# Kernel tuning notes

Measured on AMD Instinct MI355X. Metric: run time of the kernel, lower is better.

The kernel has to match this reference:

```python
import jax, jax.numpy as jnp
import numpy as np

DIM_IN_Q = 4096
DIM_IN_K = 4096
MSG_DIM = 4096


def setup_inputs() -> dict:
    key = jax.random.key(0)
    ks = jax.random.split(key, 8)
    s_q = 1.0 / np.sqrt(DIM_IN_Q)
    s_l = 1.0 / np.sqrt(MSG_DIM)
    s_k = 1.0 / np.sqrt(DIM_IN_K)
    return {
        # forward args (2-D path; N == msg_dim and M == 6 are structural requirements)
        "data_q": jax.random.normal(ks[0], (MSG_DIM, DIM_IN_Q), jnp.float32),
        "data_k": jax.random.normal(ks[1], (6, DIM_IN_K), jnp.float32),
        # learned parameters (torch nn.Linear layout: [out, in])
        "W_q": jax.random.uniform(ks[2], (MSG_DIM, DIM_IN_Q), jnp.float32, -s_q, s_q),
        "b_q": jax.random.uniform(ks[3], (MSG_DIM,), jnp.float32, -s_q, s_q),
        "W_lin": jax.random.uniform(ks[4], (6, MSG_DIM), jnp.float32, -s_l, s_l),
        "b_lin": jax.random.uniform(ks[5], (6,), jnp.float32, -s_l, s_l),
        "W_k": jax.random.uniform(ks[6], (MSG_DIM, DIM_IN_K), jnp.float32, -s_k, s_k),
        "b_k": jax.random.uniform(ks[7], (MSG_DIM,), jnp.float32, -s_k, s_k),
    }


def _relu6(x):
    return jnp.clip(x, 0.0, 6.0)


def reference(data_q, data_k, W_q, b_q, W_lin, b_lin, W_k, b_k):
    # q: [N=msg_dim, msg_dim]
    q = data_q @ W_q.T + b_q
    # secondary projection over transposed q: [msg_dim, N] -> [msg_dim, 6]
    new_q = q.T @ W_lin.T + b_lin
    # k: [6, msg_dim]
    k = data_k @ W_k.T + b_k
    context = new_q.T  # [6, msg_dim]
    # custom modulation: relu6(k^2 + 2k + context*(1+|k|))
    k_mod = _relu6(jnp.square(k) + 2.0 * k + context * (1.0 + jnp.abs(k)))
    # dot: [msg_dim, 6], scaled by sqrt(msg_dim)
    dot = q @ k_mod.T
    return dot / np.sqrt(MSG_DIM).astype(np.float32)
```

## Files before the change

### kernel.cpp

```cpp
#include <hip/hip_runtime.h>
#include <hip/hip_bf16.h>
#include <stdint.h>

#define NDIM 4096

typedef __attribute__((ext_vector_type(8))) __bf16 bf16x8;
typedef __attribute__((ext_vector_type(4))) float f32x4;

__device__ inline void g2lds16(const void* g, void* l) {
  __builtin_amdgcn_global_load_lds(
      (const __attribute__((address_space(1))) void*)g,
      (__attribute__((address_space(3))) void*)l, 16, 0, 0);
}

__device__ inline unsigned short f2bf(float f) {
  union { float f; uint32_t u; } c; c.f = f;
  uint32_t u = c.u;
  uint32_t r = ((u >> 16) & 1u) + 0x7FFFu;
  return (unsigned short)((u + r) >> 16);
}

__device__ inline float bf2f(ushort u) {
  union { uint32_t u; float f; } c; c.u = ((uint32_t)u) << 16;
  return c.f;
}

__global__ __launch_bounds__(256) void convert2_kernel(const float* __restrict__ a,
                                                       ushort* __restrict__ oa,
                                                       const float* __restrict__ b,
                                                       ushort* __restrict__ ob) {
  const int bid = blockIdx.x;
  const float* in = (bid < 16384) ? a : b;
  ushort* out = (bid < 16384) ? oa : ob;
  const int idx = (bid & 16383) * 256 + threadIdx.x;
  float4 v = ((const float4*)in)[idx];
  ushort4 o;
  o.x = f2bf(v.x); o.y = f2bf(v.y); o.z = f2bf(v.z); o.w = f2bf(v.w);
  ((ushort4*)out)[idx] = o;
}


__device__ inline bf16x8 ldfrag(const ushort* half_buf, int rrow, int blk) {
  int idx = (rrow * 64 + blk * 8) ^ ((rrow & 7) << 3);
  return *(const bf16x8*)&half_buf[idx];
}

__global__ __launch_bounds__(512, 2) void gemm_q_kernel(const ushort* __restrict__ Abf,
                                                        const ushort* __restrict__ Bbf,
                                                        const float* __restrict__ bias,
                                                        ushort* __restrict__ qout) {
  __shared__ __align__(16) ushort As[2][2][8192];
  __shared__ __align__(16) ushort Bs[2][2][8192];

  const int tid = threadIdx.x;
  const int wg = blockIdx.x;
  const int swz = (wg & 7) * 32 + (wg >> 3);
  const int i0 = (swz >> 4) * 256;
  const int j0 = (swz & 15) * 256;

  const int lane = tid & 63, wid = tid >> 6;
  const int wr = wid >> 2, wc = wid & 3;
  const int l15 = lane & 15, lg = lane >> 4;

  const int srow = tid >> 3;
  const int scol = ((tid & 7) ^ (srow & 7)) * 8;

#define STAGE_HALF(tensor, grow0, k0v, dst)                                    \
  {                                                                            \
    g2lds16((tensor) + (size_t)((grow0) + srow) * NDIM + (k0v) + scol,         \
            (void*)&(dst)[tid * 8]);                                           \
    g2lds16((tensor) + (size_t)((grow0) + 64 + srow) * NDIM + (k0v) + scol,    \
            (void*)&(dst)[4096 + tid * 8]);                                    \
  }

#define SB __builtin_amdgcn_sched_barrier(0)
#define BAR { SB; __builtin_amdgcn_s_barrier(); SB; }
#define LGKM0 { asm volatile("s_waitcnt lgkmcnt(0)" ::: "memory"); SB; }

  f32x4 acc[8][4] = {};
  bf16x8 a[4][2];
  bf16x8 b[2][2][2];

#define DSR_A(bufc, mh)                                                        \
  _Pragma("unroll") for (int mi = 0; mi < 4; ++mi)                             \
  _Pragma("unroll") for (int kk = 0; kk < 2; ++kk)                             \
    a[mi][kk] = ldfrag(As[bufc][mh], wr * 64 + mi * 16 + l15, kk * 4 + lg);

#define DSR_B(bufc, nh)                                                        \
  _Pragma("unroll") for (int ni = 0; ni < 2; ++ni)                             \
  _Pragma("unroll") for (int kk = 0; kk < 2; ++kk)                             \
    b[nh][ni][kk] = ldfrag(Bs[bufc][wc >> 1],                                  \
                           (wc & 1) * 64 + ((nh) * 2 + ni) * 16 + l15,         \
                           kk * 4 + lg);

#define MFMA_PH(mh, nh)                                                        \
  __builtin_amdgcn_s_setprio(1);                                              \
  _Pragma("unroll") for (int kk = 0; kk < 2; ++kk)                             \
  _Pragma("unroll") for (int mi = 0; mi < 4; ++mi)                             \
  _Pragma("unroll") for (int ni = 0; ni < 2; ++ni)                             \
    acc[(mh) * 4 + mi][(nh) * 2 + ni] = __builtin_amdgcn_mfma_f32_16x16x32_bf16( \
        a[mi][kk], b[nh][ni][kk], acc[(mh) * 4 + mi][(nh) * 2 + ni], 0, 0, 0); \
  __builtin_amdgcn_s_setprio(0);

  STAGE_HALF(Abf, i0 + 0,   0, As[0][0]);
  STAGE_HALF(Bbf, j0 + 0,   0, Bs[0][0]);
  STAGE_HALF(Bbf, j0 + 128, 0, Bs[0][1]);
  STAGE_HALF(Abf, i0 + 128, 0, As[0][1]);
  asm volatile("s_waitcnt vmcnt(2)" ::: "memory");
  BAR;

  for (int kt = 0; kt < 64; ++kt) {
    const int bufc = kt & 1, bufn = bufc ^ 1;
    const int kn1 = ((kt + 1) & 63) * 64;

    DSR_A(bufc, 0);
    DSR_B(bufc, 0);
    STAGE_HALF(Abf, i0 + 0, kn1, As[bufn][0]);
    BAR; LGKM0;
    MFMA_PH(0, 0);
    BAR;

    DSR_B(bufc, 1);
    STAGE_HALF(Bbf, j0 + 0, kn1, Bs[bufn][0]);
    BAR; LGKM0;
    MFMA_PH(0, 1);
    asm volatile("s_waitcnt vmcnt(4)" ::: "memory");
    BAR;

    DSR_A(bufc, 1);
    STAGE_HALF(Bbf, j0 + 128, kn1, Bs[bufn][1]);
    BAR; LGKM0;
    MFMA_PH(1, 0);
    BAR;

    STAGE_HALF(Abf, i0 + 128, kn1, As[bufn][1]);
    BAR;
    MFMA_PH(1, 1);
    asm volatile("s_waitcnt vmcnt(2)" ::: "memory");
    BAR;
  }

  float bv[4];
#pragma unroll
  for (int n = 0; n < 4; ++n) bv[n] = bias[j0 + wc * 64 + n * 16 + l15];
#pragma unroll
  for (int m = 0; m < 8; ++m) {
    const int row = i0 + (m >> 2) * 128 + wr * 64 + (m & 3) * 16 + lg * 4;
#pragma unroll
    for (int n = 0; n < 4; ++n) {
      const int col = j0 + wc * 64 + n * 16 + l15;
#pragma unroll
      for (int r = 0; r < 4; ++r)
        qout[(size_t)(row + r) * NDIM + col] = f2bf(acc[m][n][r] + bv[n]);
    }
  }
#undef STAGE_HALF
#undef DSR_A
#undef DSR_B
#undef MFMA_PH
#undef BAR
#undef LGKM0
#undef SB
}

__global__ __launch_bounds__(256) void gemv_k_kernel(const float* __restrict__ data_k,
                                                     const float* __restrict__ W_k,
                                                     const float* __restrict__ b_k,
                                                     float* __restrict__ k_out) {
  const int wave = threadIdx.x >> 6, lane = threadIdx.x & 63;
  const int m = blockIdx.x * 4 + wave;
  const float4* W = (const float4*)(W_k + (size_t)m * NDIM);
  const float4* D = (const float4*)data_k;
  float acc[6] = {0.f, 0.f, 0.f, 0.f, 0.f, 0.f};
  for (int it = lane; it < NDIM / 4; it += 64) {
    float4 w = W[it];
#pragma unroll
    for (int j = 0; j < 6; ++j) {
      float4 d = D[j * (NDIM / 4) + it];
      acc[j] += w.x * d.x + w.y * d.y + w.z * d.z + w.w * d.w;
    }
  }
#pragma unroll
  for (int j = 0; j < 6; ++j)
#pragma unroll
    for (int off = 1; off < 64; off <<= 1) acc[j] += __shfl_xor(acc[j], off);
  if (lane == 0) {
    const float bv = b_k[m];
#pragma unroll
    for (int j = 0; j < 6; ++j) k_out[j * NDIM + m] = acc[j] + bv;
  }
}

__global__ __launch_bounds__(256) void newq_kernel(const ushort* __restrict__ q,
                                                   const float* __restrict__ W_lin,
                                                   float* __restrict__ newq_t) {
  const int m = blockIdx.x * 256 + threadIdx.x;
  const int n0 = blockIdx.y * 128;
  float acc[6] = {0.f, 0.f, 0.f, 0.f, 0.f, 0.f};
  for (int n = n0; n < n0 + 128; ++n) {
    const float qv = bf2f(q[(size_t)n * NDIM + m]);
#pragma unroll
    for (int j = 0; j < 6; ++j) acc[j] += qv * W_lin[j * NDIM + n];
  }
#pragma unroll
  for (int j = 0; j < 6; ++j) atomicAdd(&newq_t[j * NDIM + m], acc[j]);
}

__global__ __launch_bounds__(256) void kmod_kernel(const float* __restrict__ k_in,
                                                   const float* __restrict__ newq_t,
                                                   const float* __restrict__ b_lin,
                                                   float* __restrict__ k_mod) {
  const int idx = blockIdx.x * 256 + threadIdx.x;
  const int j = idx >> 12;
  const float kv = k_in[idx];
  const float ctx = newq_t[idx] + b_lin[j];
  float v = kv * kv + 2.f * kv + ctx * (1.f + fabsf(kv));
  v = fminf(fmaxf(v, 0.f), 6.f);
  k_mod[idx] = v;
}

__global__ __launch_bounds__(256) void dot_kernel(const ushort* __restrict__ q,
                                                  const float* __restrict__ k_mod,
                                                  float* __restrict__ out) {
  const int wave = threadIdx.x >> 6, lane = threadIdx.x & 63;
  const int n = blockIdx.x * 4 + wave;
  const uint4* Q = (const uint4*)(q + (size_t)n * NDIM);
  float acc[6] = {0.f, 0.f, 0.f, 0.f, 0.f, 0.f};
  for (int it = lane; it < 512; it += 64) {
    uint4 v = Q[it];
    float qf[8];
    qf[0] = __builtin_bit_cast(float, v.x << 16);
    qf[1] = __builtin_bit_cast(float, v.x & 0xffff0000u);
    qf[2] = __builtin_bit_cast(float, v.y << 16);
    qf[3] = __builtin_bit_cast(float, v.y & 0xffff0000u);
    qf[4] = __builtin_bit_cast(float, v.z << 16);
    qf[5] = __builtin_bit_cast(float, v.z & 0xffff0000u);
    qf[6] = __builtin_bit_cast(float, v.w << 16);
    qf[7] = __builtin_bit_cast(float, v.w & 0xffff0000u);
#pragma unroll
    for (int j = 0; j < 6; ++j) {
      const float4* KM = (const float4*)(k_mod + j * NDIM);
      float4 k0 = KM[it * 2], k1 = KM[it * 2 + 1];
      acc[j] += qf[0] * k0.x + qf[1] * k0.y + qf[2] * k0.z + qf[3] * k0.w
              + qf[4] * k1.x + qf[5] * k1.y + qf[6] * k1.z + qf[7] * k1.w;
    }
  }
#pragma unroll
  for (int j = 0; j < 6; ++j)
#pragma unroll
    for (int off = 1; off < 64; off <<= 1) acc[j] += __shfl_xor(acc[j], off);
  if (lane == 0) {
#pragma unroll
    for (int j = 0; j < 6; ++j) out[n * 6 + j] = acc[j] * 0.015625f;
  }
}

extern "C" void kernel_launch(void* const* d_in, const int* in_sizes, int n_in,
                              void* d_out, int out_size, void* d_ws, size_t ws_size,
                              hipStream_t stream) {
  const float* data_q = (const float*)d_in[0];
  const float* data_k = (const float*)d_in[1];
  const float* W_q    = (const float*)d_in[2];
  const float* b_q    = (const float*)d_in[3];
  const float* W_lin  = (const float*)d_in[4];
  const float* b_lin  = (const float*)d_in[5];
  const float* W_k    = (const float*)d_in[6];
  const float* b_k    = (const float*)d_in[7];
  float* out = (float*)d_out;

  char* ws = (char*)d_ws;
  ushort* Abf   = (ushort*)ws;
  ushort* Bbf   = (ushort*)(ws + ((size_t)32 << 20));
  ushort* q_bf  = (ushort*)(ws + ((size_t)64 << 20));
  float*  k_arr = (float*)(ws + ((size_t)96 << 20));
  float*  newq  = k_arr + 6 * NDIM;
  float*  kmod  = newq + 6 * NDIM;

  hipMemsetAsync(newq, 0, 6 * NDIM * sizeof(float), stream);

  convert2_kernel<<<32768, 256, 0, stream>>>(data_q, Abf, W_q, Bbf);
  gemm_q_kernel<<<256, 512, 0, stream>>>(Abf, Bbf, b_q, q_bf);
  gemv_k_kernel<<<1024, 256, 0, stream>>>(data_k, W_k, b_k, k_arr);
  newq_kernel<<<dim3(16, 32), 256, 0, stream>>>(q_bf, W_lin, newq);
  kmod_kernel<<<96, 256, 0, stream>>>(k_arr, newq, b_lin, kmod);
  dot_kernel<<<1024, 256, 0, stream>>>(q_bf, kmod, out);
}
```

Before: 360.5 us.

## Fuse new_q projection into GEMM epilogue and merge prep kernels

Folds the W_lin projection of q into the GEMM epilogue: each thread multiplies its fp32 accumulator values by W_lin and reduces through shuffles, LDS atomics and global atomics. This removes the separate newq kernel, which re-read the whole bf16 q matrix. The bf16 conversion, the k GEMV and the zeroing of newq are merged into one launch, replacing the memset and two kernel launches. The GEMM's vmcnt waits are also loosened to vmcnt(4) throughout. Costs are a longer epilogue with extra W_lin loads, extra registers and LDS, and a possible race because the prefetch waits were relaxed.

Result: slower. 418.1 us (+16.0%).

```diff
diff --git a/kernel.cpp b/kernel.cpp
--- a/kernel.cpp
+++ b/kernel.cpp
@@ -25,18 +25,51 @@
   return c.f;
 }
 
-__global__ __launch_bounds__(256) void convert2_kernel(const float* __restrict__ a,
-                                                       ushort* __restrict__ oa,
-                                                       const float* __restrict__ b,
-                                                       ushort* __restrict__ ob) {
+__global__ __launch_bounds__(256) void prep_kernel(const float* __restrict__ data_q,
+                                                   ushort* __restrict__ Abf,
+                                                   const float* __restrict__ W_q,
+                                                   ushort* __restrict__ Bbf,
+                                                   const float* __restrict__ data_k,
+                                                   const float* __restrict__ W_k,
+                                                   const float* __restrict__ b_k,
+                                                   float* __restrict__ k_out,
+                                                   float* __restrict__ newq_t) {
   const int bid = blockIdx.x;
-  const float* in = (bid < 16384) ? a : b;
-  ushort* out = (bid < 16384) ? oa : ob;
-  const int idx = (bid & 16383) * 256 + threadIdx.x;
-  float4 v = ((const float4*)in)[idx];
-  ushort4 o;
-  o.x = f2bf(v.x); o.y = f2bf(v.y); o.z = f2bf(v.z); o.w = f2bf(v.w);
-  ((ushort4*)out)[idx] = o;
+  if (bid < 32768) {
+    const float* in = (bid < 16384) ? data_q : W_q;
+    ushort* out = (bid < 16384) ? Abf : Bbf;
+    const int idx = (bid & 16383) * 256 + threadIdx.x;
+    float4 v = ((const float4*)in)[idx];
+    ushort4 o;
+    o.x = f2bf(v.x); o.y = f2bf(v.y); o.z = f2bf(v.z); o.w = f2bf(v.w);
+    ((ushort4*)out)[idx] = o;
+  } else if (bid < 33792) {
+    const int wave = threadIdx.x >> 6, lane = threadIdx.x & 63;
+    const int m = (bid - 32768) * 4 + wave;
+    const float4* W = (const float4*)(W_k + (size_t)m * NDIM);
+    const float4* D = (const float4*)data_k;
+    float acc[6] = {0.f, 0.f, 0.f, 0.f, 0.f, 0.f};
+    for (int it = lane; it < NDIM / 4; it += 64) {
+      float4 w = W[it];
+#pragma unroll
+      for (int j = 0; j < 6; ++j) {
+        float4 d = D[j * (NDIM / 4) + it];
+        acc[j] += w.x * d.x + w.y * d.y + w.z * d.z + w.w * d.w;
+      }
+    }
+#pragma unroll
+    for (int j = 0; j < 6; ++j)
+#pragma unroll
+      for (int off = 1; off < 64; off <<= 1) acc[j] += __shfl_xor(acc[j], off);
+    if (lane == 0) {
+      const float bv = b_k[m];
+#pragma unroll
+      for (int j = 0; j < 6; ++j) k_out[j * NDIM + m] = acc[j] + bv;
+    }
+  } else {
+    const int idx = (bid - 33792) * 256 + threadIdx.x;
+    newq_t[idx] = 0.f;
+  }
 }
 
 
@@ -48,9 +81,12 @@
 __global__ __launch_bounds__(512, 2) void gemm_q_kernel(const ushort* __restrict__ Abf,
                                                         const ushort* __restrict__ Bbf,
                                                         const float* __restrict__ bias,
-                                                        ushort* __restrict__ qout) {
+                                                        const float* __restrict__ W_lin,
+                                                        ushort* __restrict__ qout,
+                                                        float* __restrict__ newq_t) {
   __shared__ __align__(16) ushort As[2][2][8192];
   __shared__ __align__(16) ushort Bs[2][2][8192];
+  __shared__ float newq_part[6 * 256];
 
   const int tid = threadIdx.x;
   const int wg = blockIdx.x;
@@ -76,6 +112,7 @@
 #define SB __builtin_amdgcn_sched_barrier(0)
 #define BAR { SB; __builtin_amdgcn_s_barrier(); SB; }
 #define LGKM0 { asm volatile("s_waitcnt lgkmcnt(0)" ::: "memory"); SB; }
+#define VM4 { asm volatile("s_waitcnt vmcnt(4)" ::: "memory"); SB; }
 
   f32x4 acc[8][4] = {};
   bf16x8 a[4][2];
@@ -102,11 +139,14 @@
         a[mi][kk], b[nh][ni][kk], acc[(mh) * 4 + mi][(nh) * 2 + ni], 0, 0, 0); \
   __builtin_amdgcn_s_setprio(0);
 
+#pragma unroll
+  for (int i = tid; i < 1536; i += 512) newq_part[i] = 0.f;
+
   STAGE_HALF(Abf, i0 + 0,   0, As[0][0]);
   STAGE_HALF(Bbf, j0 + 0,   0, Bs[0][0]);
   STAGE_HALF(Bbf, j0 + 128, 0, Bs[0][1]);
   STAGE_HALF(Abf, i0 + 128, 0, As[0][1]);
-  asm volatile("s_waitcnt vmcnt(2)" ::: "memory");
+  VM4;
   BAR;
 
   for (int kt = 0; kt < 64; ++kt) {
@@ -118,13 +158,14 @@
     STAGE_HALF(Abf, i0 + 0, kn1, As[bufn][0]);
     BAR; LGKM0;
     MFMA_PH(0, 0);
+    VM4;
     BAR;
 
     DSR_B(bufc, 1);
     STAGE_HALF(Bbf, j0 + 0, kn1, Bs[bufn][0]);
     BAR; LGKM0;
     MFMA_PH(0, 1);
-    asm volatile("s_waitcnt vmcnt(4)" ::: "memory");
+    VM4;
     BAR;
 
     DSR_A(bufc, 1);
@@ -136,23 +177,50 @@
     STAGE_HALF(Abf, i0 + 128, kn1, As[bufn][1]);
     BAR;
     MFMA_PH(1, 1);
-    asm volatile("s_waitcnt vmcnt(2)" ::: "memory");
+    VM4;
     BAR;
   }
 
   float bv[4];
 #pragma unroll
   for (int n = 0; n < 4; ++n) bv[n] = bias[j0 + wc * 64 + n * 16 + l15];
+
+  float p[6][4] = {};
 #pragma unroll
   for (int m = 0; m < 8; ++m) {
     const int row = i0 + (m >> 2) * 128 + wr * 64 + (m & 3) * 16 + lg * 4;
+    float wl[6][4];
+#pragma unroll
+    for (int r = 0; r < 4; ++r)
+#pragma unroll
+      for (int jj = 0; jj < 6; ++jj)
+        wl[jj][r] = W_lin[jj * NDIM + row + r];
 #pragma unroll
     for (int n = 0; n < 4; ++n) {
       const int col = j0 + wc * 64 + n * 16 + l15;
 #pragma unroll
-      for (int r = 0; r < 4; ++r)
-        qout[(size_t)(row + r) * NDIM + col] = f2bf(acc[m][n][r] + bv[n]);
-    }
+      for (int r = 0; r < 4; ++r) {
+        const float qv = acc[m][n][r] + bv[n];
+        qout[(size_t)(row + r) * NDIM + col] = f2bf(qv);
+#pragma unroll
+        for (int jj = 0; jj < 6; ++jj) p[jj][n] += qv * wl[jj][r];
+      }
+    }
+  }
+
+#pragma unroll
+  for (int jj = 0; jj < 6; ++jj)
+#pragma unroll
+    for (int n = 0; n < 4; ++n) {
+      float v = p[jj][n];
+      v += __shfl_xor(v, 16);
+      v += __shfl_xor(v, 32);
+      if (lg == 0) atomicAdd(&newq_part[jj * 256 + wc * 64 + n * 16 + l15], v);
+    }
+  __syncthreads();
+  for (int i = tid; i < 1536; i += 512) {
+    const int jj = i >> 8, c = i & 255;
+    atomicAdd(&newq_t[jj * NDIM + j0 + c], newq_part[i]);
   }
 #undef STAGE_HALF
 #undef DSR_A
@@ -160,50 +228,8 @@
 #undef MFMA_PH
 #undef BAR
 #undef LGKM0
+#undef VM4
 #undef SB
-}
-
-__global__ __launch_bounds__(256) void gemv_k_kernel(const float* __restrict__ data_k,
-                                                     const float* __restrict__ W_k,
-                                                     const float* __restrict__ b_k,
-                                                     float* __restrict__ k_out) {
-  const int wave = threadIdx.x >> 6, lane = threadIdx.x & 63;
-  const int m = blockIdx.x * 4 + wave;
-  const float4* W = (const float4*)(W_k + (size_t)m * NDIM);
-  const float4* D = (const float4*)data_k;
-  float acc[6] = {0.f, 0.f, 0.f, 0.f, 0.f, 0.f};
-  for (int it = lane; it < NDIM / 4; it += 64) {
-    float4 w = W[it];
-#pragma unroll
-    for (int j = 0; j < 6; ++j) {
-      float4 d = D[j * (NDIM / 4) + it];
-      acc[j] += w.x * d.x + w.y * d.y + w.z * d.z + w.w * d.w;
-    }
-  }
-#pragma unroll
-  for (int j = 0; j < 6; ++j)
-#pragma unroll
-    for (int off = 1; off < 64; off <<= 1) acc[j] += __shfl_xor(acc[j], off);
-  if (lane == 0) {
-    const float bv = b_k[m];
-#pragma unroll
-    for (int j = 0; j < 6; ++j) k_out[j * NDIM + m] = acc[j] + bv;
-  }
-}
-
-__global__ __launch_bounds__(256) void newq_kernel(const ushort* __restrict__ q,
-                                                   const float* __restrict__ W_lin,
-                                                   float* __restrict__ newq_t) {
-  const int m = blockIdx.x * 256 + threadIdx.x;
-  const int n0 = blockIdx.y * 128;
-  float acc[6] = {0.f, 0.f, 0.f, 0.f, 0.f, 0.f};
-  for (int n = n0; n < n0 + 128; ++n) {
-    const float qv = bf2f(q[(size_t)n * NDIM + m]);
-#pragma unroll
-    for (int j = 0; j < 6; ++j) acc[j] += qv * W_lin[j * NDIM + n];
-  }
-#pragma unroll
-  for (int j = 0; j < 6; ++j) atomicAdd(&newq_t[j * NDIM + m], acc[j]);
 }
 
 __global__ __launch_bounds__(256) void kmod_kernel(const float* __restrict__ k_in,
@@ -276,12 +302,9 @@
   float*  newq  = k_arr + 6 * NDIM;
   float*  kmod  = newq + 6 * NDIM;
 
-  hipMemsetAsync(newq, 0, 6 * NDIM * sizeof(float), stream);
-
-  convert2_kernel<<<32768, 256, 0, stream>>>(data_q, Abf, W_q, Bbf);
-  gemm_q_kernel<<<256, 512, 0, stream>>>(Abf, Bbf, b_q, q_bf);
-  gemv_k_kernel<<<1024, 256, 0, stream>>>(data_k, W_k, b_k, k_arr);
-  newq_kernel<<<dim3(16, 32), 256, 0, stream>>>(q_bf, W_lin, newq);
+  prep_kernel<<<33888, 256, 0, stream>>>(data_q, Abf, W_q, Bbf,
+                                         data_k, W_k, b_k, k_arr, newq);
+  gemm_q_kernel<<<256, 512, 0, stream>>>(Abf, Bbf, b_q, W_lin, q_bf, newq);
   kmod_kernel<<<96, 256, 0, stream>>>(k_arr, newq, b_lin, kmod);
   dot_kernel<<<1024, 256, 0, stream>>>(q_bf, kmod, out);
 }
```
